# Optimization experiments

Hardware: AMD Instinct MI355X
Metric: run time of the kernel (lower is better)

## Reference

```python
import jax, jax.numpy as jnp
import numpy as np

MIN_STATES = 4
MAX_STATES = 64
B, S, D_IN, D_ST = 32, 2048, 1024, 512


def _linear_init(k, out_dim, in_dim):
    k1, k2 = jax.random.split(k)
    s = 1.0 / np.sqrt(in_dim)
    W = jax.random.uniform(k1, (out_dim, in_dim), minval=-s, maxval=s, dtype=jnp.float32)
    b = jax.random.uniform(k2, (out_dim,), minval=-s, maxval=s, dtype=jnp.float32)
    return W, b


def setup_inputs() -> dict:
    key = jax.random.key(0)
    ks = jax.random.split(key, 8)
    # complexity estimator MLP: D_IN -> D_ST -> D_ST//2 -> 1
    W1, b1 = _linear_init(ks[0], D_ST, D_IN)
    W2, b2 = _linear_init(ks[1], D_ST // 2, D_ST)
    W3, b3 = _linear_init(ks[2], 1, D_ST // 2)
    # importance scorer MLP: D_ST -> D_ST//2 -> 1
    Ws1, bs1 = _linear_init(ks[3], D_ST // 2, D_ST)
    Ws2, bs2 = _linear_init(ks[4], 1, D_ST // 2)
    state_bank = jax.random.normal(ks[5], (MAX_STATES, D_ST), dtype=jnp.float32) * 0.02
    temperature = jnp.ones((1,), dtype=jnp.float32)
    x = jax.random.normal(ks[6], (B, S, D_IN), dtype=jnp.float32)
    return dict(x=x, W1=W1, b1=b1, W2=W2, b2=b2, W3=W3, b3=b3,
                Ws1=Ws1, bs1=bs1, Ws2=Ws2, bs2=bs2,
                state_bank=state_bank, temperature=temperature)


def reference(x, W1, b1, W2, b2, W3, b3, Ws1, bs1, Ws2, bs2, state_bank, temperature):
    # --- complexity: mean-pool over seq, 3-layer MLP with sigmoid ---
    x_pooled = x.mean(axis=1)                                   # [B, D_IN]
    h = jax.nn.relu(x_pooled @ W1.T + b1)                       # [B, D_ST]
    h = jax.nn.relu(h @ W2.T + b2)                              # [B, D_ST//2]
    complexity = jax.nn.sigmoid(h @ W3.T + b3)[:, 0]            # [B]
    # --- importance over state bank: 2-layer MLP + tempered softmax ---
    hs = jax.nn.relu(state_bank @ Ws1.T + bs1)                  # [MAX_STATES, D_ST//2]
    imp_logits = (hs @ Ws2.T + bs2)[:, 0]                       # [MAX_STATES]
    temp = jnp.maximum(jnp.abs(temperature), 0.1)[0]
    importance = jax.nn.softmax(imp_logits / temp)              # [MAX_STATES]
    # --- per-sample number of active states ---
    num_states = jnp.clip(
        jnp.round(MIN_STATES + complexity * (MAX_STATES - MIN_STATES)).astype(jnp.int32),
        MIN_STATES, MAX_STATES)                                 # [B]
    # --- vectorized top-k mask: rank of each state in descending importance ---
    order = jnp.argsort(-importance)                            # [MAX_STATES]
    ranks = jnp.argsort(order)                                  # ranks[i] = position of state i
    state_mask = ranks[None, :] < num_states[:, None]           # [B, MAX_STATES] bool
    allocated_states = jnp.broadcast_to(state_bank[None], (x.shape[0],) + state_bank.shape)
    return allocated_states, state_mask
```

## Files before the change

kernel.cpp:

```cpp
#include <hip/hip_runtime.h>

#define BB 32
#define SS 2048
#define DIN 1024
#define DST 512
#define DH 256
#define NST 64
#define SC 64
#define CHUNKS (SS / SC)
#define POOLBLKS (BB * CHUNKS)

__device__ __forceinline__ float dot4(float4 a, float4 b) {
    return a.x * b.x + a.y * b.y + a.z * b.z + a.w * b.w;
}

__global__ void kA(const float* __restrict__ x, const float* __restrict__ bank,
                   const float* __restrict__ Ws1, const float* __restrict__ bs1,
                   float* __restrict__ partial, float* __restrict__ hs,
                   float* __restrict__ out) {
    int blk = blockIdx.x, t = threadIdx.x;
    if (blk < POOLBLKS) {
        int b = blk >> 5;
        int c = blk & 31;
        const float4* xp = (const float4*)(x + ((size_t)b * SS + (size_t)c * SC) * DIN);
        float4 acc = make_float4(0.f, 0.f, 0.f, 0.f);
#pragma unroll 8
        for (int s = 0; s < SC; ++s) {
            float4 v = xp[s * (DIN / 4) + t];
            acc.x += v.x; acc.y += v.y; acc.z += v.z; acc.w += v.w;
        }
        ((float4*)(partial + (size_t)blk * DIN))[t] = acc;
    } else if (blk < POOLBLKS + 64) {
        int g = blk - POOLBLKS;
        int i = t & 63;
        int j = g * 4 + (t >> 6);
        const float4* w = (const float4*)(Ws1 + (size_t)j * DST);
        const float4* s = (const float4*)(bank + (size_t)i * DST);
        float a0 = 0.f, a1 = 0.f;
#pragma unroll 8
        for (int k = 0; k < DST / 4; k += 2) {
            a0 += dot4(w[k], s[k]);
            a1 += dot4(w[k + 1], s[k + 1]);
        }
        hs[(size_t)i * DH + j] = fmaxf(a0 + a1 + bs1[j], 0.f);
    } else {
        int idx = (blk - (POOLBLKS + 64)) * 256 + t;
        ((float4*)out)[idx] = ((const float4*)bank)[idx & 8191];
    }
}

__global__ void kB(const float* __restrict__ partial,
                   const float* __restrict__ W1, const float* __restrict__ b1,
                   const float* __restrict__ hs,
                   const float* __restrict__ Ws2, const float* __restrict__ bs2,
                   float* __restrict__ h1, float* __restrict__ imp) {
    int blk = blockIdx.x, t = threadIdx.x;
    if (blk < 128) {
        int b = blk >> 2, jc = blk & 3;
        __shared__ float4 s_pool[256];
        __shared__ float s_a[128], s_b[128];

        const float4* src = (const float4*)(partial + (size_t)b * CHUNKS * DIN);
        float4 acc = make_float4(0.f, 0.f, 0.f, 0.f);
#pragma unroll 8
        for (int c = 0; c < CHUNKS; ++c) {
            float4 v = src[c * (DIN / 4) + t];
            acc.x += v.x; acc.y += v.y; acc.z += v.z; acc.w += v.w;
        }
        const float invS = 1.0f / (float)SS;
        acc.x *= invS; acc.y *= invS; acc.z *= invS; acc.w *= invS;
        s_pool[t] = acc;
        __syncthreads();

        int jj = t & 127, half = t >> 7;
        int j = jc * 128 + jj;
        const float4* w = (const float4*)(W1 + (size_t)j * DIN) + half * 128;
        const float4* p = s_pool + half * 128;
        float d0 = 0.f, d1 = 0.f;
#pragma unroll 8
        for (int k = 0; k < 128; k += 2) {
            d0 += dot4(w[k], p[k]);
            d1 += dot4(w[k + 1], p[k + 1]);
        }
        if (half == 0) s_a[jj] = d0 + d1; else s_b[jj] = d0 + d1;
        __syncthreads();
        if (t < 128) {
            int jg = jc * 128 + t;
            h1[(size_t)b * DST + jg] = fmaxf(s_a[t] + s_b[t] + b1[jg], 0.f);
        }
    } else if (t < NST) {
        const float4* hv = (const float4*)(hs + (size_t)t * DH);
        const float4* w  = (const float4*)(Ws2);
        float a = 0.f;
#pragma unroll 8
        for (int k = 0; k < DH / 4; ++k) a += dot4(hv[k], w[k]);
        imp[t] = a + bs2[0];
    }
}

__global__ void kC(const float* __restrict__ h1,
                   const float* __restrict__ W2, const float* __restrict__ b2,
                   const float* __restrict__ W3, const float* __restrict__ b3,
                   const float* __restrict__ imp, float* __restrict__ mask_out) {
    int b = blockIdx.x, t = threadIdx.x;
    __shared__ float4 s_h[128];
    __shared__ float s_c[DH];
    __shared__ float s_imp[NST];
    __shared__ int s_ns;

    if (t < 128) s_h[t] = ((const float4*)(h1 + (size_t)b * DST))[t];
    if (t >= 128 && t < 192) s_imp[t - 128] = imp[t - 128];
    __syncthreads();

    {
        const float4* w = (const float4*)(W2 + (size_t)t * DST);
        float a0 = 0.f, a1 = 0.f;
#pragma unroll 8
        for (int k = 0; k < 128; k += 2) {
            a0 += dot4(w[k], s_h[k]);
            a1 += dot4(w[k + 1], s_h[k + 1]);
        }
        float h2v = fmaxf(a0 + a1 + b2[t], 0.f);
        s_c[t] = h2v * W3[t];
    }
    __syncthreads();

    if (t < 64) {
        float zp = s_c[t] + s_c[t + 64] + s_c[t + 128] + s_c[t + 192];
        zp += __shfl_xor(zp, 1);
        zp += __shfl_xor(zp, 2);
        zp += __shfl_xor(zp, 4);
        zp += __shfl_xor(zp, 8);
        zp += __shfl_xor(zp, 16);
        zp += __shfl_xor(zp, 32);
        if (t == 0) {
            float z = zp + b3[0];
            float cx = 1.0f / (1.0f + expf(-z));
            int ns = (int)rintf(4.0f + cx * 60.0f);
            s_ns = min(max(ns, 4), 64);
        }
    }
    __syncthreads();

    if (t < 64) {
        float mine = s_imp[t];
        int r = 0;
        for (int j2 = 0; j2 < 64; ++j2) {
            float o = s_imp[j2];
            if (o > mine || (o == mine && j2 < t)) ++r;
        }
        mask_out[b * NST + t] = (r < s_ns) ? 1.0f : 0.0f;
    }
}

extern "C" void kernel_launch(void* const* d_in, const int* in_sizes, int n_in,
                              void* d_out, int out_size, void* d_ws, size_t ws_size,
                              hipStream_t stream) {
    const float* x    = (const float*)d_in[0];
    const float* W1   = (const float*)d_in[1];
    const float* b1   = (const float*)d_in[2];
    const float* W2   = (const float*)d_in[3];
    const float* b2   = (const float*)d_in[4];
    const float* W3   = (const float*)d_in[5];
    const float* b3   = (const float*)d_in[6];
    const float* Ws1  = (const float*)d_in[7];
    const float* bs1  = (const float*)d_in[8];
    const float* Ws2  = (const float*)d_in[9];
    const float* bs2  = (const float*)d_in[10];
    const float* bank = (const float*)d_in[11];

    float* out = (float*)d_out;
    float* mask_out = out + (size_t)BB * NST * DST;

    float* ws = (float*)d_ws;
    float* partial = ws;
    float* hs  = partial + (size_t)POOLBLKS * DIN;
    float* h1  = hs + (size_t)NST * DH;
    float* imp = h1 + (size_t)BB * DST;

    kA<<<POOLBLKS + 64 + 1024, 256, 0, stream>>>(x, bank, Ws1, bs1, partial, hs, out);
    kB<<<129, 256, 0, stream>>>(partial, W1, b1, hs, Ws2, bs2, h1, imp);
    kC<<<32, 256, 0, stream>>>(h1, W2, b2, W3, b3, imp, mask_out);
}
```

Measured before the change: 107.3 us.

## Fuse MLP tail kernels into one per-batch kernel and move bank broadcast

Merges the W1 layer, importance logits, W2/W3 layers and top-k mask into a single kernel with one block per batch element, eliminating the third launch and the h1/imp round trips through global memory. The state-bank broadcast copy moves from the pooling kernel to extra blocks of the second kernel so it runs alongside the serial MLP tail. The trade-off is that the W1 matvec now runs on only 32 blocks instead of 128, so each block reads a full 2 MB of W1 with less parallelism, and every block recomputes the 64 importance logits.

```diff
diff --git a/kernel.cpp b/kernel.cpp
--- a/kernel.cpp
+++ b/kernel.cpp
@@ -16,8 +16,7 @@
 
 __global__ void kA(const float* __restrict__ x, const float* __restrict__ bank,
                    const float* __restrict__ Ws1, const float* __restrict__ bs1,
-                   float* __restrict__ partial, float* __restrict__ hs,
-                   float* __restrict__ out) {
+                   float* __restrict__ partial, float* __restrict__ hsbuf) {
     int blk = blockIdx.x, t = threadIdx.x;
     if (blk < POOLBLKS) {
         int b = blk >> 5;
@@ -30,7 +29,7 @@
             acc.x += v.x; acc.y += v.y; acc.z += v.z; acc.w += v.w;
         }
         ((float4*)(partial + (size_t)blk * DIN))[t] = acc;
-    } else if (blk < POOLBLKS + 64) {
+    } else {
         int g = blk - POOLBLKS;
         int i = t & 63;
         int j = g * 4 + (t >> 6);
@@ -42,85 +41,77 @@
             a0 += dot4(w[k], s[k]);
             a1 += dot4(w[k + 1], s[k + 1]);
         }
-        hs[(size_t)i * DH + j] = fmaxf(a0 + a1 + bs1[j], 0.f);
-    } else {
-        int idx = (blk - (POOLBLKS + 64)) * 256 + t;
-        ((float4*)out)[idx] = ((const float4*)bank)[idx & 8191];
+        hsbuf[(size_t)i * DH + j] = fmaxf(a0 + a1 + bs1[j], 0.f);
     }
 }
 
-__global__ void kB(const float* __restrict__ partial,
-                   const float* __restrict__ W1, const float* __restrict__ b1,
-                   const float* __restrict__ hs,
-                   const float* __restrict__ Ws2, const float* __restrict__ bs2,
-                   float* __restrict__ h1, float* __restrict__ imp) {
+__global__ __launch_bounds__(256) void kB(
+        const float* __restrict__ partial,
+        const float* __restrict__ W1, const float* __restrict__ b1,
+        const float* __restrict__ W2, const float* __restrict__ b2,
+        const float* __restrict__ W3, const float* __restrict__ b3,
+        const float* __restrict__ hsbuf,
+        const float* __restrict__ Ws2, const float* __restrict__ bs2,
+        const float* __restrict__ bank,
+        float* __restrict__ out, float* __restrict__ mask_out) {
     int blk = blockIdx.x, t = threadIdx.x;
-    if (blk < 128) {
-        int b = blk >> 2, jc = blk & 3;
-        __shared__ float4 s_pool[256];
-        __shared__ float s_a[128], s_b[128];
+    if (blk >= BB) {
+        int idx = (blk - BB) * 256 + t;
+        ((float4*)out)[idx] = ((const float4*)bank)[idx & 8191];
+        return;
+    }
+    int b = blk;
+    __shared__ float4 s_pool[256];
+    __shared__ float s_h1[DST];
+    __shared__ float s_c[DH];
+    __shared__ float s_imp[NST];
+    __shared__ int s_ns;
 
-        const float4* src = (const float4*)(partial + (size_t)b * CHUNKS * DIN);
-        float4 acc = make_float4(0.f, 0.f, 0.f, 0.f);
+    const float4* src = (const float4*)(partial + (size_t)b * CHUNKS * DIN);
+    float4 acc = make_float4(0.f, 0.f, 0.f, 0.f);
 #pragma unroll 8
-        for (int c = 0; c < CHUNKS; ++c) {
-            float4 v = src[c * (DIN / 4) + t];
-            acc.x += v.x; acc.y += v.y; acc.z += v.z; acc.w += v.w;
-        }
-        const float invS = 1.0f / (float)SS;
-        acc.x *= invS; acc.y *= invS; acc.z *= invS; acc.w *= invS;
-        s_pool[t] = acc;
-        __syncthreads();
+    for (int c = 0; c < CHUNKS; ++c) {
+        float4 v = src[c * (DIN / 4) + t];
+        acc.x += v.x; acc.y += v.y; acc.z += v.z; acc.w += v.w;
+    }
+    const float invS = 1.0f / (float)SS;
+    acc.x *= invS; acc.y *= invS; acc.z *= invS; acc.w *= invS;
+    s_pool[t] = acc;
 
-        int jj = t & 127, half = t >> 7;
-        int j = jc * 128 + jj;
-        const float4* w = (const float4*)(W1 + (size_t)j * DIN) + half * 128;
-        const float4* p = s_pool + half * 128;
-        float d0 = 0.f, d1 = 0.f;
-#pragma unroll 8
-        for (int k = 0; k < 128; k += 2) {
-            d0 += dot4(w[k], p[k]);
-            d1 += dot4(w[k + 1], p[k + 1]);
-        }
-        if (half == 0) s_a[jj] = d0 + d1; else s_b[jj] = d0 + d1;
-        __syncthreads();
-        if (t < 128) {
-            int jg = jc * 128 + t;
-            h1[(size_t)b * DST + jg] = fmaxf(s_a[t] + s_b[t] + b1[jg], 0.f);
-        }
-    } else if (t < NST) {
-        const float4* hv = (const float4*)(hs + (size_t)t * DH);
+    if (t < NST) {
+        const float4* hv = (const float4*)(hsbuf + (size_t)t * DH);
         const float4* w  = (const float4*)(Ws2);
         float a = 0.f;
 #pragma unroll 8
         for (int k = 0; k < DH / 4; ++k) a += dot4(hv[k], w[k]);
-        imp[t] = a + bs2[0];
+        s_imp[t] = a + bs2[0];
     }
-}
+    __syncthreads();
 
-__global__ void kC(const float* __restrict__ h1,
-                   const float* __restrict__ W2, const float* __restrict__ b2,
-                   const float* __restrict__ W3, const float* __restrict__ b3,
-                   const float* __restrict__ imp, float* __restrict__ mask_out) {
-    int b = blockIdx.x, t = threadIdx.x;
-    __shared__ float4 s_h[128];
-    __shared__ float s_c[DH];
-    __shared__ float s_imp[NST];
-    __shared__ int s_ns;
-
-    if (t < 128) s_h[t] = ((const float4*)(h1 + (size_t)b * DST))[t];
-    if (t >= 128 && t < 192) s_imp[t - 128] = imp[t - 128];
+#pragma unroll
+    for (int p = 0; p < 2; ++p) {
+        int j = p * 256 + t;
+        const float4* w = (const float4*)(W1 + (size_t)j * DIN);
+        float d0 = 0.f, d1 = 0.f;
+#pragma unroll 16
+        for (int k = 0; k < DIN / 4; k += 2) {
+            d0 += dot4(w[k], s_pool[k]);
+            d1 += dot4(w[k + 1], s_pool[k + 1]);
+        }
+        s_h1[j] = fmaxf(d0 + d1 + b1[j], 0.f);
+    }
     __syncthreads();
 
     {
         const float4* w = (const float4*)(W2 + (size_t)t * DST);
-        float a0 = 0.f, a1 = 0.f;
-#pragma unroll 8
-        for (int k = 0; k < 128; k += 2) {
-            a0 += dot4(w[k], s_h[k]);
-            a1 += dot4(w[k + 1], s_h[k + 1]);
+        const float4* hv = (const float4*)s_h1;
+        float d0 = 0.f, d1 = 0.f;
+#pragma unroll 16
+        for (int k = 0; k < DST / 4; k += 2) {
+            d0 += dot4(w[k], hv[k]);
+            d1 += dot4(w[k + 1], hv[k + 1]);
         }
-        float h2v = fmaxf(a0 + a1 + b2[t], 0.f);
+        float h2v = fmaxf(d0 + d1 + b2[t], 0.f);
         s_c[t] = h2v * W3[t];
     }
     __syncthreads();
@@ -174,11 +165,9 @@
 
     float* ws = (float*)d_ws;
     float* partial = ws;
-    float* hs  = partial + (size_t)POOLBLKS * DIN;
-    float* h1  = hs + (size_t)NST * DH;
-    float* imp = h1 + (size_t)BB * DST;
+    float* hsbuf = partial + (size_t)POOLBLKS * DIN;
 
-    kA<<<POOLBLKS + 64 + 1024, 256, 0, stream>>>(x, bank, Ws1, bs1, partial, hs, out);
-    kB<<<129, 256, 0, stream>>>(partial, W1, b1, hs, Ws2, bs2, h1, imp);
-    kC<<<32, 256, 0, stream>>>(h1, W2, b2, W3, b3, imp, mask_out);
+    kA<<<POOLBLKS + 64, 256, 0, stream>>>(x, bank, Ws1, bs1, partial, hsbuf);
+    kB<<<BB + 1024, 256, 0, stream>>>(partial, W1, b1, W2, b2, W3, b3,
+                                      hsbuf, Ws2, bs2, bank, out, mask_out);
 }
```

Result: slower. 152.3 us (+41.9%).
